# Optimization experiments

Measured on AMD Instinct MI355X. Metric: run time of the kernel, lower is better.

The kernel has to match this reference:

```python
import jax, jax.numpy as jnp
import numpy as np

B, S, IN, HID, HEADS, TRAITS = 128, 32, 32, 128, 8, 10


def setup_inputs() -> dict:
    key = jax.random.key(0)
    ks = jax.random.split(key, 40)
    f32 = jnp.float32
    def W(k, shape, s=0.02):
        return (jax.random.normal(k, shape, f32) * s)
    path = jax.random.normal(ks[0], (B, S, IN), f32)
    # monotonically increasing shared time grid (timestamps[0] is what cdeint uses)
    dt = jax.random.uniform(ks[1], (S,), f32, 0.05, 0.15)
    ts = jnp.broadcast_to(jnp.cumsum(dt), (B, S))
    inp = {
        "interaction_path": path,
        "timestamps": ts,
        # initial encoder: Linear(IN,HID) -> LN -> GELU -> Linear(HID,HID) -> LN
        "enc_W1": W(ks[2], (IN, HID)), "enc_b1": jnp.zeros((HID,), f32),
        "enc_g1": jnp.ones((HID,), f32), "enc_bt1": jnp.zeros((HID,), f32),
        "enc_W2": W(ks[3], (HID, HID)), "enc_b2": jnp.zeros((HID,), f32),
        "enc_g2": jnp.ones((HID,), f32), "enc_bt2": jnp.zeros((HID,), f32),
        # vector field: Linear(HID,2HID)->LN->GELU -> Linear(2HID,2HID)->LN->GELU -> Linear(2HID,HID*IN)
        "vf_W1": W(ks[4], (HID, 2 * HID)), "vf_b1": jnp.zeros((2 * HID,), f32),
        "vf_g1": jnp.ones((2 * HID,), f32), "vf_bt1": jnp.zeros((2 * HID,), f32),
        "vf_W2": W(ks[5], (2 * HID, 2 * HID)), "vf_b2": jnp.zeros((2 * HID,), f32),
        "vf_g2": jnp.ones((2 * HID,), f32), "vf_bt2": jnp.zeros((2 * HID,), f32),
        "vf_W3": W(ks[6], (2 * HID, HID * IN), 0.005), "vf_b3": jnp.zeros((HID * IN,), f32),
        # MultiheadAttention (q=k=v, single token)
        "Wq": W(ks[7], (HID, HID)), "bq": jnp.zeros((HID,), f32),
        "Wk": W(ks[8], (HID, HID)), "bk": jnp.zeros((HID,), f32),
        "Wv": W(ks[9], (HID, HID)), "bv": jnp.zeros((HID,), f32),
        "Wo": W(ks[10], (HID, HID)), "bo": jnp.zeros((HID,), f32),
        # trait decoder (2-layer MLP -> TRAITS)
        "dec_W1": W(ks[11], (HID, HID)), "dec_b1": jnp.zeros((HID,), f32),
        "dec_W2": W(ks[12], (HID, TRAITS)), "dec_b2": jnp.zeros((TRAITS,), f32),
    }
    return inp


def reference(interaction_path, timestamps,
              enc_W1, enc_b1, enc_g1, enc_bt1, enc_W2, enc_b2, enc_g2, enc_bt2,
              vf_W1, vf_b1, vf_g1, vf_bt1, vf_W2, vf_b2, vf_g2, vf_bt2, vf_W3, vf_b3,
              Wq, bq, Wk, bk, Wv, bv, Wo, bo,
              dec_W1, dec_b1, dec_W2, dec_b2):
    b, s, in_dim = interaction_path.shape
    hid = enc_W1.shape[1]
    nh = HEADS
    dh = hid // nh

    def ln(x, g, bb):
        mu = jnp.mean(x, -1, keepdims=True)
        v = jnp.mean((x - mu) ** 2, -1, keepdims=True)
        return (x - mu) / jnp.sqrt(v + 1e-5) * g + bb

    gelu = lambda x: jax.nn.gelu(x, approximate=False)

    # initial encoder on first time point (dropout = eval mode)
    x0 = interaction_path[:, 0]
    h0 = gelu(ln(x0 @ enc_W1 + enc_b1, enc_g1, enc_bt1))
    z0 = ln(h0 @ enc_W2 + enc_b2, enc_g2, enc_bt2)  # [B, HID]

    # linear-interpolation control path: piecewise-constant derivative per interval
    dts = timestamps[:, 1:] - timestamps[:, :-1]                       # [B, S-1]
    dX = (interaction_path[:, 1:] - interaction_path[:, :-1]) / dts[..., None]  # [B, S-1, IN]

    def vf(z):
        h = gelu(ln(z @ vf_W1 + vf_b1, vf_g1, vf_bt1))
        h = gelu(ln(h @ vf_W2 + vf_b2, vf_g2, vf_bt2))
        return (h @ vf_W3 + vf_b3).reshape(z.shape[0], hid, in_dim)    # [B, HID, IN]

    def drift(z, dxdt):
        return jnp.einsum('bhi,bi->bh', vf(z), dxdt)

    def rk4_step(z, inp):
        dxdt, hstep = inp               # [B, IN], [B]
        hb = hstep[:, None]
        k1 = drift(z, dxdt)
        k2 = drift(z + 0.5 * hb * k1, dxdt)
        k3 = drift(z + 0.5 * hb * k2, dxdt)
        k4 = drift(z + hb * k3, dxdt)
        z_next = z + (hb / 6.0) * (k1 + 2 * k2 + 2 * k3 + k4)
        return z_next, None

    zT, _ = jax.lax.scan(rk4_step, z0, (jnp.swapaxes(dX, 0, 1), dts.T))  # [B, HID]

    # single-token self-attention (softmax over one key -> weights = 1)
    q = (zT @ Wq + bq).reshape(b, nh, dh)
    k = (zT @ Wk + bk).reshape(b, nh, dh)
    v = (zT @ Wv + bv).reshape(b, nh, dh)
    scores = jnp.sum(q * k, -1, keepdims=True) / jnp.sqrt(jnp.float32(dh))  # [B, nh, 1]
    w = jax.nn.softmax(scores[..., None], axis=-1)                           # [B, nh, 1, 1] == 1
    attn = (w[..., 0] * v).reshape(b, hid)
    final = attn @ Wo + bo
    attention_weights = jnp.mean(w, axis=1)  # [B, 1, 1] averaged over heads (torch default)

    hD = gelu(final @ dec_W1 + dec_b1)
    traits = hD @ dec_W2 + dec_b2            # [B, TRAITS]
    return traits, attention_weights
```

## Files before the change

### kernel.cpp

```cpp
#include <hip/hip_runtime.h>
#include <hip/hip_bf16.h>

#define BB 128
#define SS 32
#define NSTEP 31
#define IND 32
#define HID 128
#define HID2 256

typedef unsigned short u16;
typedef unsigned int u32;
typedef _Float16 f16;
typedef f16 h2 __attribute__((ext_vector_type(2)));
typedef __fp16 fp16v2 __attribute__((ext_vector_type(2)));
typedef _Float16 f16x8 __attribute__((ext_vector_type(8)));
typedef float f32x4 __attribute__((ext_vector_type(4)));

__device__ __forceinline__ float dot2f(u32 a, u32 b, float c){
#if __has_builtin(__builtin_amdgcn_fdot2)
  h2 ha, hb; __builtin_memcpy(&ha, &a, 4); __builtin_memcpy(&hb, &b, 4);
  return __builtin_amdgcn_fdot2(ha, hb, c, false);
#else
  h2 ha, hb; __builtin_memcpy(&ha, &a, 4); __builtin_memcpy(&hb, &b, 4);
  return c + (float)ha[0]*(float)hb[0] + (float)ha[1]*(float)hb[1];
#endif
}
__device__ __forceinline__ u32 pkh2(float a, float b){
  fp16v2 r = __builtin_amdgcn_cvt_pkrtz(a, b);
  u32 u; __builtin_memcpy(&u, &r, 4); return u;
}
__device__ __forceinline__ u16 f2h(float f){ f16 h = (f16)f; u16 u; __builtin_memcpy(&u, &h, 2); return u; }
__device__ __forceinline__ float gelu_f(float x){ return 0.5f * x * (1.0f + erff(x * 0.70710678118654752440f)); }

__device__ __forceinline__ float wred(float v){
  int iv; float tf;
  #define DPPADD(CTRL, RMASK) \
    __builtin_memcpy(&iv, &v, 4); \
    iv = __builtin_amdgcn_update_dpp(0, iv, CTRL, RMASK, 0xf, true); \
    __builtin_memcpy(&tf, &iv, 4); \
    v += tf;
  DPPADD(0x111, 0xf)
  DPPADD(0x112, 0xf)
  DPPADD(0x114, 0xf)
  DPPADD(0x118, 0xf)
  DPPADD(0x142, 0xa)
  DPPADD(0x143, 0xc)
  #undef DPPADD
  return v;
}

__device__ __forceinline__ void bsum2(float x, float y, float* red, int tid, float& ox, float& oy){
  #pragma unroll
  for (int off = 32; off >= 1; off >>= 1){ x += __shfl_xor(x, off); y += __shfl_xor(y, off); }
  __syncthreads();
  if ((tid & 63) == 0){ red[(tid >> 6)*2] = x; red[(tid >> 6)*2 + 1] = y; }
  __syncthreads();
  ox = red[0] + red[2] + red[4] + red[6];
  oy = red[1] + red[3] + red[5] + red[7];
}

__global__ __launch_bounds__(128) void prep_misc(const float* __restrict__ path,
                                                 const float* __restrict__ ts,
                                                 const float* __restrict__ b3,
                                                 u32* __restrict__ dxh,
                                                 float* __restrict__ hb,
                                                 float* __restrict__ gb){
  const int b = blockIdx.x, tid = threadIdx.x;
  __shared__ float sdxp[NSTEP * IND];
  for (int t = tid; t < NSTEP * IND; t += 128){
    int s = t >> 5, i = t & 31;
    float dt = ts[b*SS + s + 1] - ts[b*SS + s];
    sdxp[t] = (path[(b*SS + s + 1)*IND + i] - path[(b*SS + s)*IND + i]) / dt;
  }
  if (tid < NSTEP) hb[b*NSTEP + tid] = ts[b*SS + tid + 1] - ts[b*SS + tid];
  __syncthreads();
  for (int t = tid; t < NSTEP * 16; t += 128){
    int s = t >> 4, i2 = t & 15;
    dxh[((size_t)b*NSTEP + s)*16 + i2] = pkh2(sdxp[s*IND + 2*i2], sdxp[s*IND + 2*i2 + 1]);
  }
  if (tid < HID){
    float w[IND];
    #pragma unroll
    for (int i = 0; i < IND; ++i) w[i] = b3[tid*IND + i];
    for (int s = 0; s < NSTEP; ++s){
      float a = 0.f;
      #pragma unroll
      for (int i = 0; i < IND; ++i) a = fmaf(w[i], sdxp[s*IND + i], a);
      gb[(b*NSTEP + s)*HID + tid] = a;
    }
  }
}

__global__ __launch_bounds__(256) void pack_w3(const float* __restrict__ W3, u32* __restrict__ w3h){
  int i = blockIdx.x*256 + threadIdx.x;
  if (i < (HID2*HID*IND)/2) w3h[i] = pkh2(W3[2*i], W3[2*i + 1]);
}

__global__ __launch_bounds__(256) void pack_wf(const float* __restrict__ W1,
                                               const float* __restrict__ W2,
                                               u32* __restrict__ w1f,
                                               u32* __restrict__ w2f){
  int i = blockIdx.x*256 + threadIdx.x;
  if (i < 16384){
    int lane_blk = i >> 6, rem = i & 63;
    int i16 = rem >> 2, q = rem & 3;
    int w = lane_blk >> 6, lane = lane_blk & 63;
    int kt = i16 >> 2, nt = i16 & 3;
    int k = kt*32 + (lane >> 4)*8 + 2*q;
    int col = w*64 + nt*16 + (lane & 15);
    w1f[i] = pkh2(W1[(size_t)k*HID2 + col], W1[(size_t)(k+1)*HID2 + col]);
  } else if (i < 16384 + 32768){
    int j = i - 16384;
    int lane_blk = j >> 7, rem = j & 127;
    int i32i = rem >> 2, q = rem & 3;
    int w = lane_blk >> 6, lane = lane_blk & 63;
    int kt = i32i >> 2, nt = i32i & 3;
    int k = kt*32 + (lane >> 4)*8 + 2*q;
    int col = w*64 + nt*16 + (lane & 15);
    w2f[j] = pkh2(W2[(size_t)k*HID2 + col], W2[(size_t)(k+1)*HID2 + col]);
  }
}

struct FusedP {
  const float *path;
  const float *eW1,*eb1,*eg1,*ebt1,*eW2,*eb2,*eg2,*ebt2;
  const u32 *w1f, *w2f;
  const float *b1,*g1,*bt1,*b2,*g2,*bt2;
  const float *Wv,*bv,*Wo,*bo,*dW1,*db1,*dW2,*db2;
  const float *hb,*gb;
  const u32 *Gp;
  float *zstate, *out;
  int s0, s1, do_enc, do_epi, scan_on;
  const u32 *w3h, *dxh;
  u32 *Gpw;
  int ps0, pcs;
};

__global__ __launch_bounds__(256, 1) void fused_kernel(FusedP p){
  const int tid = threadIdx.x;
  __shared__ __align__(16) u16 zst_h[HID];
  __shared__ __align__(16) u16 a1p_h[HID2];
  __shared__ __align__(16) u16 a2p_h[HID2];
  __shared__ __align__(16) float red[8];
  __shared__ __align__(16) float zf[HID];
  __shared__ __align__(16) float sc1[HID2];
  __shared__ u32 sdx[BB * 16];

  if (p.scan_on && blockIdx.x < BB){
    const int b = blockIdx.x;
    const int lane = tid & 63, w = tid >> 6;
    const int quad = lane >> 4, n16 = lane & 15;
    const bool owner = (quad == 0);

    uint4 w1r[16], w2r[32];
    {
      const uint4* s1p = (const uint4*)p.w1f + ((size_t)(w*64 + lane))*16;
      #pragma unroll
      for (int i = 0; i < 16; ++i) w1r[i] = s1p[i];
      const uint4* s2p = (const uint4*)p.w2f + ((size_t)(w*64 + lane))*32;
      #pragma unroll
      for (int i = 0; i < 32; ++i) w2r[i] = s2p[i];
    }
    float rb1[4], rg1[4], rbt1[4], rb2[4], rg2[4], rbt2[4];
    #pragma unroll
    for (int nt = 0; nt < 4; ++nt){
      int col = w*64 + nt*16 + n16;
      rb1[nt] = p.b1[col]; rg1[nt] = p.g1[col]; rbt1[nt] = p.bt1[col];
      rb2[nt] = p.b2[col]; rg2[nt] = p.g2[col]; rbt2[nt] = p.bt2[col];
    }
    const int h0 = w*32 + n16, h1 = h0 + 16;

    float mu, sq;
    if (p.do_enc){
      if (tid < IND) sc1[tid] = p.path[(b*SS + 0)*IND + tid];
      __syncthreads();
      float acc = 0.f;
      if (tid < HID){
        acc = p.eb1[tid];
        #pragma unroll 8
        for (int i = 0; i < IND; ++i) acc = fmaf(sc1[i], p.eW1[i*HID + tid], acc);
      }
      float cx = (tid < HID) ? acc : 0.f;
      bsum2(cx, cx*cx, red, tid, mu, sq);
      mu *= (1.f/HID); float var = sq*(1.f/HID) - mu*mu; float rstd = rsqrtf(var + 1e-5f);
      if (tid < HID) zf[tid] = gelu_f((acc - mu)*rstd*p.eg1[tid] + p.ebt1[tid]);
      __syncthreads();
      float acc2 = 0.f;
      if (tid < HID){
        acc2 = p.eb2[tid];
        #pragma unroll 8
        for (int h = 0; h < HID; ++h) acc2 = fmaf(zf[h], p.eW2[h*HID + tid], acc2);
      }
      cx = (tid < HID) ? acc2 : 0.f;
      bsum2(cx, cx*cx, red, tid, mu, sq);
      mu *= (1.f/HID); float var2 = sq*(1.f/HID) - mu*mu; float rstd2 = rsqrtf(var2 + 1e-5f);
      __syncthreads();
      if (tid < HID) zf[tid] = (acc2 - mu)*rstd2*p.eg2[tid] + p.ebt2[tid];
      __syncthreads();
    }
    float zc0 = 0.f, zc1 = 0.f;
    if (owner){
      if (p.do_enc){ zc0 = zf[h0]; zc1 = zf[h1]; }
      else { zc0 = p.zstate[b*HID + h0]; zc1 = p.zstate[b*HID + h1]; }
    }

    for (int s = p.s0; s < p.s1; ++s){
      const float hbv = p.hb[b*NSTEP + s];
      uint4 gr[16];
      {
        const uint4* g4 = (const uint4*)(p.Gp + ((size_t)(s - p.s0)*BB + b)*16384 + (size_t)w*4096);
        #pragma unroll
        for (int m = 0; m < 16; ++m) gr[m] = g4[m*64 + lane];
      }
      float gb0 = 0.f, gb1 = 0.f;
      if (owner){
        gb0 = p.gb[(b*NSTEP + s)*HID + h0];
        gb1 = p.gb[(b*NSTEP + s)*HID + h1];
        zst_h[h0] = f2h(zc0); zst_h[h1] = f2h(zc1);
      }
      float ks0 = 0.f, ks1 = 0.f;
      __syncthreads();

      #pragma unroll 1
      for (int st = 0; st < 4; ++st){
        f32x4 D0 = {0,0,0,0}, D1 = {0,0,0,0}, D2 = {0,0,0,0}, D3 = {0,0,0,0};
        {
          const uint4* za = (const uint4*)zst_h;
          #pragma unroll
          for (int kt = 0; kt < 4; ++kt){
            f16x8 a; uint4 av = za[kt*4 + quad]; __builtin_memcpy(&a, &av, 16);
            f16x8 bf;
            __builtin_memcpy(&bf, &w1r[kt*4+0], 16); D0 = __builtin_amdgcn_mfma_f32_16x16x32_f16(a, bf, D0, 0, 0, 0);
            __builtin_memcpy(&bf, &w1r[kt*4+1], 16); D1 = __builtin_amdgcn_mfma_f32_16x16x32_f16(a, bf, D1, 0, 0, 0);
            __builtin_memcpy(&bf, &w1r[kt*4+2], 16); D2 = __builtin_amdgcn_mfma_f32_16x16x32_f16(a, bf, D2, 0, 0, 0);
            __builtin_memcpy(&bf, &w1r[kt*4+3], 16); D3 = __builtin_amdgcn_mfma_f32_16x16x32_f16(a, bf, D3, 0, 0, 0);
          }
        }
        float v0 = D0[0] + rb1[0], v1 = D1[0] + rb1[1], v2 = D2[0] + rb1[2], v3 = D3[0] + rb1[3];
        float ssum = wred((v0 + v1) + (v2 + v3));
        float ssq  = wred((v0*v0 + v1*v1) + (v2*v2 + v3*v3));
        if (lane == 63){ red[w*2] = ssum; red[w*2+1] = ssq; }
        __syncthreads();
        {
          const float4* r4 = (const float4*)red;
          float4 ra = r4[0], rb = r4[1];
          float m1 = (ra.x + ra.z + rb.x + rb.z)*(1.f/1024.f);
          float q1 = (ra.y + ra.w + rb.y + rb.w)*(1.f/1024.f);
          float rs1 = rsqrtf(q1 - m1*m1 + 1e-5f);
          if (owner){
            a1p_h[w*64 +  0 + n16] = f2h(gelu_f((v0 - m1)*rs1*rg1[0] + rbt1[0]));
            a1p_h[w*64 + 16 + n16] = f2h(gelu_f((v1 - m1)*rs1*rg1[1] + rbt1[1]));
            a1p_h[w*64 + 32 + n16] = f2h(gelu_f((v2 - m1)*rs1*rg1[2] + rbt1[2]));
            a1p_h[w*64 + 48 + n16] = f2h(gelu_f((v3 - m1)*rs1*rg1[3] + rbt1[3]));
          }
        }
        __syncthreads();
        D0 = {0,0,0,0}; D1 = {0,0,0,0}; D2 = {0,0,0,0}; D3 = {0,0,0,0};
        {
          const uint4* aa = (const uint4*)a1p_h;
          #pragma unroll
          for (int kt = 0; kt < 8; ++kt){
            f16x8 a; uint4 av = aa[kt*4 + quad]; __builtin_memcpy(&a, &av, 16);
            f16x8 bf;
            __builtin_memcpy(&bf, &w2r[kt*4+0], 16); D0 = __builtin_amdgcn_mfma_f32_16x16x32_f16(a, bf, D0, 0, 0, 0);
            __builtin_memcpy(&bf, &w2r[kt*4+1], 16); D1 = __builtin_amdgcn_mfma_f32_16x16x32_f16(a, bf, D1, 0, 0, 0);
            __builtin_memcpy(&bf, &w2r[kt*4+2], 16); D2 = __builtin_amdgcn_mfma_f32_16x16x32_f16(a, bf, D2, 0, 0, 0);
            __builtin_memcpy(&bf, &w2r[kt*4+3], 16); D3 = __builtin_amdgcn_mfma_f32_16x16x32_f16(a, bf, D3, 0, 0, 0);
          }
        }
        v0 = D0[0] + rb2[0]; v1 = D1[0] + rb2[1]; v2 = D2[0] + rb2[2]; v3 = D3[0] + rb2[3];
        ssum = wred((v0 + v1) + (v2 + v3));
        ssq  = wred((v0*v0 + v1*v1) + (v2*v2 + v3*v3));
        if (lane == 63){ red[w*2] = ssum; red[w*2+1] = ssq; }
        __syncthreads();
        {
          const float4* r4 = (const float4*)red;
          float4 ra = r4[0], rb = r4[1];
          float m2 = (ra.x + ra.z + rb.x + rb.z)*(1.f/1024.f);
          float q2 = (ra.y + ra.w + rb.y + rb.w)*(1.f/1024.f);
          float rs2 = rsqrtf(q2 - m2*m2 + 1e-5f);
          if (owner){
            a2p_h[w*64 +  0 + n16] = f2h(gelu_f((v0 - m2)*rs2*rg2[0] + rbt2[0]));
            a2p_h[w*64 + 16 + n16] = f2h(gelu_f((v1 - m2)*rs2*rg2[1] + rbt2[1]));
            a2p_h[w*64 + 32 + n16] = f2h(gelu_f((v2 - m2)*rs2*rg2[2] + rbt2[2]));
            a2p_h[w*64 + 48 + n16] = f2h(gelu_f((v3 - m2)*rs2*rg2[3] + rbt2[3]));
          }
        }
        __syncthreads();
        f32x4 E0 = {0,0,0,0}, E1 = {0,0,0,0};
        {
          const uint4* aa = (const uint4*)a2p_h;
          #pragma unroll
          for (int kt = 0; kt < 8; ++kt){
            f16x8 a; uint4 av = aa[kt*4 + quad]; __builtin_memcpy(&a, &av, 16);
            f16x8 g0f, g1f;
            __builtin_memcpy(&g0f, &gr[kt*2+0], 16);
            __builtin_memcpy(&g1f, &gr[kt*2+1], 16);
            E0 = __builtin_amdgcn_mfma_f32_16x16x32_f16(a, g0f, E0, 0, 0, 0);
            E1 = __builtin_amdgcn_mfma_f32_16x16x32_f16(a, g1f, E1, 0, 0, 0);
          }
        }
        if (owner){
          float kv0 = E0[0] + gb0, kv1 = E1[0] + gb1;
          float cst = (st == 0 || st == 3) ? 1.f : 2.f;
          ks0 += cst*kv0; ks1 += cst*kv1;
          if (st < 3){
            float c = (st == 2) ? hbv : 0.5f*hbv;
            zst_h[h0] = f2h(zc0 + c*kv0);
            zst_h[h1] = f2h(zc1 + c*kv1);
          }
        }
        __syncthreads();
      }
      if (owner){ zc0 += hbv*(1.f/6.f)*ks0; zc1 += hbv*(1.f/6.f)*ks1; }
    }

    if (p.do_epi){
      if (owner){ zf[h0] = zc0; zf[h1] = zc1; }
      __syncthreads();
      if (tid < HID){
        float v = p.bv[tid];
        #pragma unroll 8
        for (int h = 0; h < HID; ++h) v = fmaf(zf[h], p.Wv[h*HID + tid], v);
        sc1[tid] = v;
      }
      __syncthreads();
      if (tid < HID){
        float f = p.bo[tid];
        #pragma unroll 8
        for (int h = 0; h < HID; ++h) f = fmaf(sc1[h], p.Wo[h*HID + tid], f);
        sc1[HID + tid] = f;
      }
      __syncthreads();
      if (tid < HID){
        float hd = p.db1[tid];
        #pragma unroll 8
        for (int h = 0; h < HID; ++h) hd = fmaf(sc1[HID + h], p.dW1[h*HID + tid], hd);
        zf[tid] = gelu_f(hd);
      }
      __syncthreads();
      if (tid < 10){
        float t = p.db2[tid];
        #pragma unroll 8
        for (int h = 0; h < HID; ++h) t = fmaf(zf[h], p.dW2[h*10 + tid], t);
        p.out[b*10 + tid] = t;
      }
      if (tid == 0) p.out[BB*10 + b] = 1.0f;
    } else {
      if (owner){ p.zstate[b*HID + h0] = zc0; p.zstate[b*HID + h1] = zc1; }
    }
    return;
  }

  {
    const int pb = blockIdx.x - (p.scan_on ? BB : 0);
    const int sl = pb >> 6, xblk = pb & 63;
    if (sl >= p.pcs) return;
    const int s = p.ps0 + sl;
    const int lin = xblk*256 + tid;
    const int kp = lin >> 7, h = lin & 127;
    const uint4* wa = (const uint4*)(p.w3h + ((size_t)(2*kp)*HID + h)*16);
    const uint4* wb = (const uint4*)(p.w3h + ((size_t)(2*kp+1)*HID + h)*16);
    uint4 A0 = wa[0], A1 = wa[1], A2 = wa[2], A3 = wa[3];
    uint4 B0 = wb[0], B1 = wb[1], B2 = wb[2], B3 = wb[3];
    for (int t = tid; t < BB * 16; t += 256){
      int bb = t >> 4, i2 = t & 15;
      sdx[t] = p.dxh[((size_t)bb*NSTEP + s)*16 + i2];
    }
    __syncthreads();
    const int kt = kp >> 4, q = kp & 3, quad2 = (kp >> 2) & 3;
    const int wq = h >> 5, tq = (h >> 4) & 1, nn = h & 15;
    const size_t off = (size_t)wq*4096 + (size_t)(kt*2 + tq)*256 + (size_t)(quad2*16 + nn)*4 + q;
    const size_t base_sl = (size_t)sl * BB * 16384;
    u32* __restrict__ Gout = p.Gpw;
    for (int bb = 0; bb < BB; ++bb){
      const uint4* dp = (const uint4*)&sdx[bb*16];
      uint4 D0 = dp[0], D1 = dp[1], D2 = dp[2], D3 = dp[3];
      float g0 = 0.f, g1 = 0.f, g2 = 0.f, g3 = 0.f;
      g0 = dot2f(D0.x, A0.x, g0); g0 = dot2f(D0.y, A0.y, g0);
      g0 = dot2f(D0.z, A0.z, g0); g0 = dot2f(D0.w, A0.w, g0);
      g2 = dot2f(D1.x, A1.x, g2); g2 = dot2f(D1.y, A1.y, g2);
      g2 = dot2f(D1.z, A1.z, g2); g2 = dot2f(D1.w, A1.w, g2);
      g0 = dot2f(D2.x, A2.x, g0); g0 = dot2f(D2.y, A2.y, g0);
      g0 = dot2f(D2.z, A2.z, g0); g0 = dot2f(D2.w, A2.w, g0);
      g2 = dot2f(D3.x, A3.x, g2); g2 = dot2f(D3.y, A3.y, g2);
      g2 = dot2f(D3.z, A3.z, g2); g2 = dot2f(D3.w, A3.w, g2);
      g1 = dot2f(D0.x, B0.x, g1); g1 = dot2f(D0.y, B0.y, g1);
      g1 = dot2f(D0.z, B0.z, g1); g1 = dot2f(D0.w, B0.w, g1);
      g3 = dot2f(D1.x, B1.x, g3); g3 = dot2f(D1.y, B1.y, g3);
      g3 = dot2f(D1.z, B1.z, g3); g3 = dot2f(D1.w, B1.w, g3);
      g1 = dot2f(D2.x, B2.x, g1); g1 = dot2f(D2.y, B2.y, g1);
      g1 = dot2f(D2.z, B2.z, g1); g1 = dot2f(D2.w, B2.w, g1);
      g3 = dot2f(D3.x, B3.x, g3); g3 = dot2f(D3.y, B3.y, g3);
      g3 = dot2f(D3.z, B3.z, g3); g3 = dot2f(D3.w, B3.w, g3);
      Gout[base_sl + (size_t)bb*16384 + off] = pkh2(g0 + g2, g1 + g3);
    }
  }
}

extern "C" void kernel_launch(void* const* d_in, const int* in_sizes, int n_in,
                              void* d_out, int out_size, void* d_ws, size_t ws_size,
                              hipStream_t stream){
  const float* path  = (const float*)d_in[0];
  const float* ts    = (const float*)d_in[1];
  const float* eW1   = (const float*)d_in[2];
  const float* eb1   = (const float*)d_in[3];
  const float* eg1   = (const float*)d_in[4];
  const float* ebt1  = (const float*)d_in[5];
  const float* eW2   = (const float*)d_in[6];
  const float* eb2   = (const float*)d_in[7];
  const float* eg2   = (const float*)d_in[8];
  const float* ebt2  = (const float*)d_in[9];
  const float* vW1   = (const float*)d_in[10];
  const float* vb1   = (const float*)d_in[11];
  const float* vg1   = (const float*)d_in[12];
  const float* vbt1  = (const float*)d_in[13];
  const float* vW2   = (const float*)d_in[14];
  const float* vb2   = (const float*)d_in[15];
  const float* vg2   = (const float*)d_in[16];
  const float* vbt2  = (const float*)d_in[17];
  const float* vW3   = (const float*)d_in[18];
  const float* vb3   = (const float*)d_in[19];
  const float* Wv    = (const float*)d_in[24];
  const float* bv    = (const float*)d_in[25];
  const float* Wo    = (const float*)d_in[26];
  const float* bo    = (const float*)d_in[27];
  const float* dW1   = (const float*)d_in[28];
  const float* db1   = (const float*)d_in[29];
  const float* dW2   = (const float*)d_in[30];
  const float* db2   = (const float*)d_in[31];

  char* wsb = (char*)d_ws;
  float* z_state = (float*)(wsb + 0);
  u32*   dxh = (u32*)(wsb + 65536);
  float* hb  = (float*)(wsb + 319488);
  float* gb  = (float*)(wsb + 335872);
  u32*   w3h = (u32*)(wsb + 2367488);
  u32*   w1f = (u32*)(wsb + 4464640);
  u32*   w2f = (u32*)(wsb + 4530176);
  const size_t gbase = 4661248;

  hipLaunchKernelGGL(prep_misc, dim3(BB), dim3(128), 0, stream, path, ts, vb3, dxh, hb, gb);
  hipLaunchKernelGGL(pack_w3, dim3(2048), dim3(256), 0, stream, vW3, w3h);
  hipLaunchKernelGGL(pack_wf, dim3(192), dim3(256), 0, stream, vW1, vW2, w1f, w2f);

  const size_t per_step = (size_t)BB * 16384 * 4;
  size_t avail = (ws_size > gbase) ? (ws_size - gbase) : 0;
  int pipelined, c;
  int capp = (int)((avail/2) / per_step);
  if (capp >= 2){
    pipelined = 1;
    c = capp < 8 ? capp : 8;
    if (c > NSTEP) c = NSTEP;
  } else {
    pipelined = 0;
    c = (int)(avail / per_step);
    if (c < 1) c = 1;
    if (c > NSTEP) c = NSTEP;
  }
  const int nch = (NSTEP + c - 1) / c;
  u32* GpA = (u32*)(wsb + gbase);
  u32* GpB = (u32*)(wsb + gbase + (size_t)c*per_step);

  FusedP base;
  base.path = path;
  base.eW1 = eW1; base.eb1 = eb1; base.eg1 = eg1; base.ebt1 = ebt1;
  base.eW2 = eW2; base.eb2 = eb2; base.eg2 = eg2; base.ebt2 = ebt2;
  base.w1f = w1f; base.w2f = w2f;
  base.b1 = vb1; base.g1 = vg1; base.bt1 = vbt1;
  base.b2 = vb2; base.g2 = vg2; base.bt2 = vbt2;
  base.Wv = Wv; base.bv = bv; base.Wo = Wo; base.bo = bo;
  base.dW1 = dW1; base.db1 = db1; base.dW2 = dW2; base.db2 = db2;
  base.hb = hb; base.gb = gb;
  base.zstate = z_state; base.out = (float*)d_out;
  base.w3h = w3h; base.dxh = dxh;
  base.Gp = GpA; base.Gpw = GpA;
  base.s0 = 0; base.s1 = 0; base.do_enc = 0; base.do_epi = 0; base.scan_on = 0;
  base.ps0 = 0; base.pcs = 0;

  if (pipelined){
    for (int i = 0; i <= nch; ++i){
      FusedP P = base;
      int scan_i = i - 1, prep_i = i;
      P.scan_on = (scan_i >= 0) ? 1 : 0;
      if (P.scan_on){
        P.s0 = scan_i*c;
        P.s1 = (P.s0 + c < NSTEP) ? (P.s0 + c) : NSTEP;
        P.Gp = (scan_i & 1) ? GpB : GpA;
        P.do_enc = (scan_i == 0) ? 1 : 0;
        P.do_epi = (P.s1 == NSTEP) ? 1 : 0;
      }
      if (prep_i < nch){
        P.ps0 = prep_i*c;
        P.pcs = (NSTEP - P.ps0 < c) ? (NSTEP - P.ps0) : c;
        P.Gpw = (prep_i & 1) ? GpB : GpA;
      } else {
        P.pcs = 0;
      }
      int grid = (P.scan_on ? BB : 0) + 64*P.pcs;
      if (grid == 0) continue;
      hipLaunchKernelGGL(fused_kernel, dim3(grid), dim3(256), 0, stream, P);
    }
  } else {
    for (int i = 0; i < nch; ++i){
      int s0 = i*c;
      int cs = (NSTEP - s0 < c) ? (NSTEP - s0) : c;
      FusedP P1 = base;
      P1.scan_on = 0; P1.ps0 = s0; P1.pcs = cs; P1.Gpw = GpA;
      hipLaunchKernelGGL(fused_kernel, dim3(64*cs), dim3(256), 0, stream, P1);
      FusedP P2 = base;
      P2.scan_on = 1; P2.pcs = 0;
      P2.s0 = s0; P2.s1 = s0 + cs; P2.Gp = GpA;
      P2.do_enc = (s0 == 0) ? 1 : 0;
      P2.do_epi = (s0 + cs == NSTEP) ? 1 : 0;
      hipLaunchKernelGGL(fused_kernel, dim3(BB), dim3(256), 0, stream, P2);
    }
  }
}
```

Measured before the change: 541.8 us.

## Merge setup kernels, raise scan-block priority, split MFMA accumulator chains

Result: faster. 521.5 us (-3.7%).

```diff
diff --git a/kernel.cpp b/kernel.cpp
--- a/kernel.cpp
+++ b/kernel.cpp
@@ -31,6 +31,16 @@
 }
 __device__ __forceinline__ u16 f2h(float f){ f16 h = (f16)f; u16 u; __builtin_memcpy(&u, &h, 2); return u; }
 __device__ __forceinline__ float gelu_f(float x){ return 0.5f * x * (1.0f + erff(x * 0.70710678118654752440f)); }
+__device__ __forceinline__ void setprio_hi(){
+#if __has_builtin(__builtin_amdgcn_s_setprio)
+  __builtin_amdgcn_s_setprio(3);
+#endif
+}
+__device__ __forceinline__ void setprio_lo(){
+#if __has_builtin(__builtin_amdgcn_s_setprio)
+  __builtin_amdgcn_s_setprio(0);
+#endif
+}
 
 __device__ __forceinline__ float wred(float v){
   int iv; float tf;
@@ -59,65 +69,67 @@
   oy = red[1] + red[3] + red[5] + red[7];
 }
 
-__global__ __launch_bounds__(128) void prep_misc(const float* __restrict__ path,
-                                                 const float* __restrict__ ts,
-                                                 const float* __restrict__ b3,
-                                                 u32* __restrict__ dxh,
-                                                 float* __restrict__ hb,
-                                                 float* __restrict__ gb){
-  const int b = blockIdx.x, tid = threadIdx.x;
-  __shared__ float sdxp[NSTEP * IND];
-  for (int t = tid; t < NSTEP * IND; t += 128){
-    int s = t >> 5, i = t & 31;
-    float dt = ts[b*SS + s + 1] - ts[b*SS + s];
-    sdxp[t] = (path[(b*SS + s + 1)*IND + i] - path[(b*SS + s)*IND + i]) / dt;
-  }
-  if (tid < NSTEP) hb[b*NSTEP + tid] = ts[b*SS + tid + 1] - ts[b*SS + tid];
-  __syncthreads();
-  for (int t = tid; t < NSTEP * 16; t += 128){
-    int s = t >> 4, i2 = t & 15;
-    dxh[((size_t)b*NSTEP + s)*16 + i2] = pkh2(sdxp[s*IND + 2*i2], sdxp[s*IND + 2*i2 + 1]);
-  }
-  if (tid < HID){
-    float w[IND];
-    #pragma unroll
-    for (int i = 0; i < IND; ++i) w[i] = b3[tid*IND + i];
-    for (int s = 0; s < NSTEP; ++s){
-      float a = 0.f;
+__global__ __launch_bounds__(256) void setup_kernel(const float* __restrict__ path,
+                                                    const float* __restrict__ ts,
+                                                    const float* __restrict__ b3,
+                                                    const float* __restrict__ W3,
+                                                    const float* __restrict__ W1,
+                                                    const float* __restrict__ W2,
+                                                    u32* __restrict__ dxh,
+                                                    float* __restrict__ hb,
+                                                    float* __restrict__ gb,
+                                                    u32* __restrict__ w3h,
+                                                    u32* __restrict__ w1f,
+                                                    u32* __restrict__ w2f){
+  const int blk = blockIdx.x, tid = threadIdx.x;
+  if (blk < BB){
+    const int b = blk;
+    __shared__ float sdxp[NSTEP * IND];
+    for (int t = tid; t < NSTEP * IND; t += 256){
+      int s = t >> 5, i = t & 31;
+      float dt = ts[b*SS + s + 1] - ts[b*SS + s];
+      sdxp[t] = (path[(b*SS + s + 1)*IND + i] - path[(b*SS + s)*IND + i]) / dt;
+    }
+    if (tid < NSTEP) hb[b*NSTEP + tid] = ts[b*SS + tid + 1] - ts[b*SS + tid];
+    __syncthreads();
+    for (int t = tid; t < NSTEP * 16; t += 256){
+      int s = t >> 4, i2 = t & 15;
+      dxh[((size_t)b*NSTEP + s)*16 + i2] = pkh2(sdxp[s*IND + 2*i2], sdxp[s*IND + 2*i2 + 1]);
+    }
+    if (tid < HID){
+      float w[IND];
       #pragma unroll
-      for (int i = 0; i < IND; ++i) a = fmaf(w[i], sdxp[s*IND + i], a);
-      gb[(b*NSTEP + s)*HID + tid] = a;
-    }
-  }
-}
-
-__global__ __launch_bounds__(256) void pack_w3(const float* __restrict__ W3, u32* __restrict__ w3h){
-  int i = blockIdx.x*256 + threadIdx.x;
-  if (i < (HID2*HID*IND)/2) w3h[i] = pkh2(W3[2*i], W3[2*i + 1]);
-}
-
-__global__ __launch_bounds__(256) void pack_wf(const float* __restrict__ W1,
-                                               const float* __restrict__ W2,
-                                               u32* __restrict__ w1f,
-                                               u32* __restrict__ w2f){
-  int i = blockIdx.x*256 + threadIdx.x;
-  if (i < 16384){
-    int lane_blk = i >> 6, rem = i & 63;
-    int i16 = rem >> 2, q = rem & 3;
-    int w = lane_blk >> 6, lane = lane_blk & 63;
-    int kt = i16 >> 2, nt = i16 & 3;
-    int k = kt*32 + (lane >> 4)*8 + 2*q;
-    int col = w*64 + nt*16 + (lane & 15);
-    w1f[i] = pkh2(W1[(size_t)k*HID2 + col], W1[(size_t)(k+1)*HID2 + col]);
-  } else if (i < 16384 + 32768){
-    int j = i - 16384;
-    int lane_blk = j >> 7, rem = j & 127;
-    int i32i = rem >> 2, q = rem & 3;
-    int w = lane_blk >> 6, lane = lane_blk & 63;
-    int kt = i32i >> 2, nt = i32i & 3;
-    int k = kt*32 + (lane >> 4)*8 + 2*q;
-    int col = w*64 + nt*16 + (lane & 15);
-    w2f[j] = pkh2(W2[(size_t)k*HID2 + col], W2[(size_t)(k+1)*HID2 + col]);
+      for (int i = 0; i < IND; ++i) w[i] = b3[tid*IND + i];
+      for (int s = 0; s < NSTEP; ++s){
+        float a = 0.f;
+        #pragma unroll
+        for (int i = 0; i < IND; ++i) a = fmaf(w[i], sdxp[s*IND + i], a);
+        gb[(b*NSTEP + s)*HID + tid] = a;
+      }
+    }
+  } else if (blk < BB + 2048){
+    int i = (blk - BB)*256 + tid;
+    if (i < (HID2*HID*IND)/2) w3h[i] = pkh2(W3[2*i], W3[2*i + 1]);
+  } else {
+    int i = (blk - BB - 2048)*256 + tid;
+    if (i < 16384){
+      int lane_blk = i >> 6, rem = i & 63;
+      int i16 = rem >> 2, q = rem & 3;
+      int w = lane_blk >> 6, lane = lane_blk & 63;
+      int kt = i16 >> 2, nt = i16 & 3;
+      int k = kt*32 + (lane >> 4)*8 + 2*q;
+      int col = w*64 + nt*16 + (lane & 15);
+      w1f[i] = pkh2(W1[(size_t)k*HID2 + col], W1[(size_t)(k+1)*HID2 + col]);
+    } else if (i < 16384 + 32768){
+      int j = i - 16384;
+      int lane_blk = j >> 7, rem = j & 127;
+      int i32i = rem >> 2, q = rem & 3;
+      int w = lane_blk >> 6, lane = lane_blk & 63;
+      int kt = i32i >> 2, nt = i32i & 3;
+      int k = kt*32 + (lane >> 4)*8 + 2*q;
+      int col = w*64 + nt*16 + (lane & 15);
+      w2f[j] = pkh2(W2[(size_t)k*HID2 + col], W2[(size_t)(k+1)*HID2 + col]);
+    }
   }
 }
 
@@ -147,6 +159,7 @@
   __shared__ u32 sdx[BB * 16];
 
   if (p.scan_on && blockIdx.x < BB){
+    setprio_hi();
     const int b = blockIdx.x;
     const int lane = tid & 63, w = tid >> 6;
     const int quad = lane >> 4, n16 = lane & 15;
@@ -223,20 +236,31 @@
 
       #pragma unroll 1
       for (int st = 0; st < 4; ++st){
-        f32x4 D0 = {0,0,0,0}, D1 = {0,0,0,0}, D2 = {0,0,0,0}, D3 = {0,0,0,0};
+        f32x4 D0a={0,0,0,0}, D1a={0,0,0,0}, D2a={0,0,0,0}, D3a={0,0,0,0};
+        f32x4 D0b={0,0,0,0}, D1b={0,0,0,0}, D2b={0,0,0,0}, D3b={0,0,0,0};
         {
           const uint4* za = (const uint4*)zst_h;
           #pragma unroll
-          for (int kt = 0; kt < 4; ++kt){
+          for (int kt = 0; kt < 2; ++kt){
             f16x8 a; uint4 av = za[kt*4 + quad]; __builtin_memcpy(&a, &av, 16);
             f16x8 bf;
-            __builtin_memcpy(&bf, &w1r[kt*4+0], 16); D0 = __builtin_amdgcn_mfma_f32_16x16x32_f16(a, bf, D0, 0, 0, 0);
-            __builtin_memcpy(&bf, &w1r[kt*4+1], 16); D1 = __builtin_amdgcn_mfma_f32_16x16x32_f16(a, bf, D1, 0, 0, 0);
-            __builtin_memcpy(&bf, &w1r[kt*4+2], 16); D2 = __builtin_amdgcn_mfma_f32_16x16x32_f16(a, bf, D2, 0, 0, 0);
-            __builtin_memcpy(&bf, &w1r[kt*4+3], 16); D3 = __builtin_amdgcn_mfma_f32_16x16x32_f16(a, bf, D3, 0, 0, 0);
+            __builtin_memcpy(&bf, &w1r[kt*4+0], 16); D0a = __builtin_amdgcn_mfma_f32_16x16x32_f16(a, bf, D0a, 0, 0, 0);
+            __builtin_memcpy(&bf, &w1r[kt*4+1], 16); D1a = __builtin_amdgcn_mfma_f32_16x16x32_f16(a, bf, D1a, 0, 0, 0);
+            __builtin_memcpy(&bf, &w1r[kt*4+2], 16); D2a = __builtin_amdgcn_mfma_f32_16x16x32_f16(a, bf, D2a, 0, 0, 0);
+            __builtin_memcpy(&bf, &w1r[kt*4+3], 16); D3a = __builtin_amdgcn_mfma_f32_16x16x32_f16(a, bf, D3a, 0, 0, 0);
+          }
+          #pragma unroll
+          for (int kt = 2; kt < 4; ++kt){
+            f16x8 a; uint4 av = za[kt*4 + quad]; __builtin_memcpy(&a, &av, 16);
+            f16x8 bf;
+            __builtin_memcpy(&bf, &w1r[kt*4+0], 16); D0b = __builtin_amdgcn_mfma_f32_16x16x32_f16(a, bf, D0b, 0, 0, 0);
+            __builtin_memcpy(&bf, &w1r[kt*4+1], 16); D1b = __builtin_amdgcn_mfma_f32_16x16x32_f16(a, bf, D1b, 0, 0, 0);
+            __builtin_memcpy(&bf, &w1r[kt*4+2], 16); D2b = __builtin_amdgcn_mfma_f32_16x16x32_f16(a, bf, D2b, 0, 0, 0);
+            __builtin_memcpy(&bf, &w1r[kt*4+3], 16); D3b = __builtin_amdgcn_mfma_f32_16x16x32_f16(a, bf, D3b, 0, 0, 0);
           }
         }
-        float v0 = D0[0] + rb1[0], v1 = D1[0] + rb1[1], v2 = D2[0] + rb1[2], v3 = D3[0] + rb1[3];
+        float v0 = (D0a[0]+D0b[0]) + rb1[0], v1 = (D1a[0]+D1b[0]) + rb1[1];
+        float v2 = (D2a[0]+D2b[0]) + rb1[2], v3 = (D3a[0]+D3b[0]) + rb1[3];
         float ssum = wred((v0 + v1) + (v2 + v3));
         float ssq  = wred((v0*v0 + v1*v1) + (v2*v2 + v3*v3));
         if (lane == 63){ red[w*2] = ssum; red[w*2+1] = ssq; }
@@ -255,20 +279,31 @@
           }
         }
         __syncthreads();
-        D0 = {0,0,0,0}; D1 = {0,0,0,0}; D2 = {0,0,0,0}; D3 = {0,0,0,0};
+        D0a={0,0,0,0}; D1a={0,0,0,0}; D2a={0,0,0,0}; D3a={0,0,0,0};
+        D0b={0,0,0,0}; D1b={0,0,0,0}; D2b={0,0,0,0}; D3b={0,0,0,0};
         {
           const uint4* aa = (const uint4*)a1p_h;
           #pragma unroll
-          for (int kt = 0; kt < 8; ++kt){
+          for (int kt = 0; kt < 4; ++kt){
             f16x8 a; uint4 av = aa[kt*4 + quad]; __builtin_memcpy(&a, &av, 16);
             f16x8 bf;
-            __builtin_memcpy(&bf, &w2r[kt*4+0], 16); D0 = __builtin_amdgcn_mfma_f32_16x16x32_f16(a, bf, D0, 0, 0, 0);
-            __builtin_memcpy(&bf, &w2r[kt*4+1], 16); D1 = __builtin_amdgcn_mfma_f32_16x16x32_f16(a, bf, D1, 0, 0, 0);
-            __builtin_memcpy(&bf, &w2r[kt*4+2], 16); D2 = __builtin_amdgcn_mfma_f32_16x16x32_f16(a, bf, D2, 0, 0, 0);
-            __builtin_memcpy(&bf, &w2r[kt*4+3], 16); D3 = __builtin_amdgcn_mfma_f32_16x16x32_f16(a, bf, D3, 0, 0, 0);
+            __builtin_memcpy(&bf, &w2r[kt*4+0], 16); D0a = __builtin_amdgcn_mfma_f32_16x16x32_f16(a, bf, D0a, 0, 0, 0);
+            __builtin_memcpy(&bf, &w2r[kt*4+1], 16); D1a = __builtin_amdgcn_mfma_f32_16x16x32_f16(a, bf, D1a, 0, 0, 0);
+            __builtin_memcpy(&bf, &w2r[kt*4+2], 16); D2a = __builtin_amdgcn_mfma_f32_16x16x32_f16(a, bf, D2a, 0, 0, 0);
+            __builtin_memcpy(&bf, &w2r[kt*4+3], 16); D3a = __builtin_amdgcn_mfma_f32_16x16x32_f16(a, bf, D3a, 0, 0, 0);
+          }
+          #pragma unroll
+          for (int kt = 4; kt < 8; ++kt){
+            f16x8 a; uint4 av = aa[kt*4 + quad]; __builtin_memcpy(&a, &av, 16);
+            f16x8 bf;
+            __builtin_memcpy(&bf, &w2r[kt*4+0], 16); D0b = __builtin_amdgcn_mfma_f32_16x16x32_f16(a, bf, D0b, 0, 0, 0);
+            __builtin_memcpy(&bf, &w2r[kt*4+1], 16); D1b = __builtin_amdgcn_mfma_f32_16x16x32_f16(a, bf, D1b, 0, 0, 0);
+            __builtin_memcpy(&bf, &w2r[kt*4+2], 16); D2b = __builtin_amdgcn_mfma_f32_16x16x32_f16(a, bf, D2b, 0, 0, 0);
+            __builtin_memcpy(&bf, &w2r[kt*4+3], 16); D3b = __builtin_amdgcn_mfma_f32_16x16x32_f16(a, bf, D3b, 0, 0, 0);
           }
         }
-        v0 = D0[0] + rb2[0]; v1 = D1[0] + rb2[1]; v2 = D2[0] + rb2[2]; v3 = D3[0] + rb2[3];
+        v0 = (D0a[0]+D0b[0]) + rb2[0]; v1 = (D1a[0]+D1b[0]) + rb2[1];
+        v2 = (D2a[0]+D2b[0]) + rb2[2]; v3 = (D3a[0]+D3b[0]) + rb2[3];
         ssum = wred((v0 + v1) + (v2 + v3));
         ssq  = wred((v0*v0 + v1*v1) + (v2*v2 + v3*v3));
         if (lane == 63){ red[w*2] = ssum; red[w*2+1] = ssq; }
@@ -287,11 +322,11 @@
           }
         }
         __syncthreads();
-        f32x4 E0 = {0,0,0,0}, E1 = {0,0,0,0};
+        f32x4 E0={0,0,0,0}, E1={0,0,0,0}, E2={0,0,0,0}, E3={0,0,0,0};
         {
           const uint4* aa = (const uint4*)a2p_h;
           #pragma unroll
-          for (int kt = 0; kt < 8; ++kt){
+          for (int kt = 0; kt < 4; ++kt){
             f16x8 a; uint4 av = aa[kt*4 + quad]; __builtin_memcpy(&a, &av, 16);
             f16x8 g0f, g1f;
             __builtin_memcpy(&g0f, &gr[kt*2+0], 16);
@@ -299,9 +334,18 @@
             E0 = __builtin_amdgcn_mfma_f32_16x16x32_f16(a, g0f, E0, 0, 0, 0);
             E1 = __builtin_amdgcn_mfma_f32_16x16x32_f16(a, g1f, E1, 0, 0, 0);
           }
+          #pragma unroll
+          for (int kt = 4; kt < 8; ++kt){
+            f16x8 a; uint4 av = aa[kt*4 + quad]; __builtin_memcpy(&a, &av, 16);
+            f16x8 g0f, g1f;
+            __builtin_memcpy(&g0f, &gr[kt*2+0], 16);
+            __builtin_memcpy(&g1f, &gr[kt*2+1], 16);
+            E2 = __builtin_amdgcn_mfma_f32_16x16x32_f16(a, g0f, E2, 0, 0, 0);
+            E3 = __builtin_amdgcn_mfma_f32_16x16x32_f16(a, g1f, E3, 0, 0, 0);
+          }
         }
         if (owner){
-          float kv0 = E0[0] + gb0, kv1 = E1[0] + gb1;
+          float kv0 = (E0[0] + E2[0]) + gb0, kv1 = (E1[0] + E3[0]) + gb1;
           float cst = (st == 0 || st == 3) ? 1.f : 2.f;
           ks0 += cst*kv0; ks1 += cst*kv1;
           if (st < 3){
@@ -353,6 +397,7 @@
   }
 
   {
+    setprio_lo();
     const int pb = blockIdx.x - (p.scan_on ? BB : 0);
     const int sl = pb >> 6, xblk = pb & 63;
     if (sl >= p.pcs) return;
@@ -440,9 +485,8 @@
   u32*   w2f = (u32*)(wsb + 4530176);
   const size_t gbase = 4661248;
 
-  hipLaunchKernelGGL(prep_misc, dim3(BB), dim3(128), 0, stream, path, ts, vb3, dxh, hb, gb);
-  hipLaunchKernelGGL(pack_w3, dim3(2048), dim3(256), 0, stream, vW3, w3h);
-  hipLaunchKernelGGL(pack_wf, dim3(192), dim3(256), 0, stream, vW1, vW2, w1f, w2f);
+  hipLaunchKernelGGL(setup_kernel, dim3(BB + 2048 + 192), dim3(256), 0, stream,
+                     path, ts, vb3, vW3, vW1, vW2, dxh, hb, gb, w3h, w1f, w2f);
 
   const size_t per_step = (size_t)BB * 16384 * 4;
   size_t avail = (ws_size > gbase) ? (ws_size - gbase) : 0;
```
